# Kernel optimization log

Measured on AMD Instinct MI355X. Metric: run time of the kernel, lower is better.

The kernel has to match this reference:

```python
import jax, jax.numpy as jnp
import numpy as np

B, T, X, H, Z = 64, 2048, 128, 256, 64


def setup_inputs() -> dict:
    key = jax.random.key(0)
    ks = jax.random.split(key, 6)
    s = lambda n: 1.0 / np.sqrt(n).astype(np.float32)
    return {
        "x_seq": jax.random.normal(ks[0], (B, T, X), jnp.float32),
        # LSTMCell params packed as [i|f|g|o] gates. Flax: input dense has no bias,
        # hidden dense has bias.
        "Wi": jax.random.normal(ks[1], (X, 4 * H), jnp.float32) * s(X),
        "Wh": jax.random.normal(ks[2], (H, 4 * H), jnp.float32) * s(H),
        "bh": jnp.zeros((4 * H,), jnp.float32),
        # head: Dense(H) -> relu -> Dense(2Z)
        "W1": jax.random.normal(ks[3], (H, H), jnp.float32) * s(H),
        "b1": jnp.zeros((H,), jnp.float32),
        "W2": jax.random.normal(ks[4], (H, 2 * Z), jnp.float32) * s(H),
        "b2": jnp.zeros((2 * Z,), jnp.float32),
    }


def _forward(x_seq, Wi, Wh, bh, W1, b1, W2, b2):
    Bsz = x_seq.shape[0]
    Hd = Wh.shape[0]
    # Precompute input projection for all timesteps (one big GEMM).
    x_proj = jnp.einsum('btx,xg->btg', x_seq, Wi)  # (B, T, 4H)
    xp = jnp.swapaxes(x_proj, 0, 1)  # (T, B, 4H) for scan

    def step(carry, xp_t):
        c, h = carry
        gates = xp_t + h @ Wh + bh  # (B, 4H)
        i, f, g, o = jnp.split(gates, 4, axis=-1)
        i = jax.nn.sigmoid(i)
        f = jax.nn.sigmoid(f)
        g = jnp.tanh(g)
        o = jax.nn.sigmoid(o)
        c = f * c + i * g
        h = o * jnp.tanh(c)
        hid = jax.nn.relu(h @ W1 + b1)
        out = hid @ W2 + b2  # (B, 2Z)
        return (c, h), out

    c0 = jnp.zeros((Bsz, Hd), x_seq.dtype)
    h0 = jnp.zeros((Bsz, Hd), x_seq.dtype)
    _, outs = jax.lax.scan(step, (c0, h0), xp)  # outs: (T, B, 2Z)
    outs = jnp.swapaxes(outs, 0, 1)  # (B, T, 2Z)
    mu_seq, log_sigma_seq = jnp.split(outs, 2, axis=-1)
    return mu_seq, log_sigma_seq


def reference(x_seq, Wi, Wh, bh, W1, b1, W2, b2):
    return _forward(x_seq, Wi, Wh, bh, W1, b1, W2, b2)
```

## Files before the change

### kernel.cpp

```cpp
#include <hip/hip_runtime.h>

typedef _Float16 f16;
typedef _Float16 h2 __attribute__((ext_vector_type(2)));
typedef _Float16 h8 __attribute__((ext_vector_type(8)));
typedef float f4 __attribute__((ext_vector_type(4)));

constexpr int Bb = 64, Tt = 2048, Xx = 128, Hh = 256, G4 = 1024, Z2 = 128;

__device__ __forceinline__ float fdot2f(h2 a, h2 b, float c) {
#if __has_builtin(__builtin_amdgcn_fdot2)
  return __builtin_amdgcn_fdot2(a, b, c, false);
#else
  return c + (float)a[0] * (float)b[0] + (float)a[1] * (float)b[1];
#endif
}
__device__ __forceinline__ float tanhf_(float x) {
  float e = __expf(2.0f * x);
  return 1.0f - 2.0f * __builtin_amdgcn_rcpf(e + 1.0f);
}
__device__ __forceinline__ h2 bch2(unsigned int u) { return __builtin_bit_cast(h2, u); }

template <int CTRL>
__device__ __forceinline__ float qb(float v) {
  return __builtin_bit_cast(float,
      __builtin_amdgcn_mov_dpp(__builtin_bit_cast(int, v), CTRL, 0xf, 0xf, true));
}
__device__ __forceinline__ float qsum(float v) {
  v += qb<0xB1>(v);
  v += qb<0x4E>(v);
  return v;
}

__global__ void cast_f16_k(const float* __restrict__ in, f16* __restrict__ out, int n) {
  int i = (blockIdx.x * 256 + threadIdx.x) * 4;
  if (i >= n) return;
  float4 v = *(const float4*)(in + i);
  h2 a = {(f16)v.x, (f16)v.y};
  h2 b = {(f16)v.z, (f16)v.w};
  uint2 o = {__builtin_bit_cast(unsigned int, a), __builtin_bit_cast(unsigned int, b)};
  *(uint2*)(out + i) = o;
}

__global__ void cast_whT_k(const float* __restrict__ Wh, f16* __restrict__ WhT) {
  int idx = blockIdx.x * 256 + threadIdx.x;
  int tid = idx >> 8, r = idx & 255;
  int s = r >> 1, e = r & 1;
  int half = s >> 6, gate = (s >> 4) & 3, kk = s & 15;
  int j = tid >> 2, q = tid & 3;
  int k = q * 64 + half * 32 + kk * 2 + e;
  WhT[idx] = (f16)Wh[(long)k * G4 + gate * 256 + j];
}

__global__ void cast_whT2_k(const float* __restrict__ Wh, f16* __restrict__ WhT2) {
  int idx = blockIdx.x * 256 + threadIdx.x;
  int tid = idx >> 9, f = idx & 511;
  int s = f >> 1, e = f & 1;
  int c_off, k;
  if (s < 96)      { c_off = 0; k = 2 * s + e; }
  else if (s < 192){ c_off = 1; k = 2 * (s - 96) + e; }
  else if (s < 224){ c_off = 0; k = 192 + 2 * (s - 192) + e; }
  else             { c_off = 1; k = 192 + 2 * (s - 224) + e; }
  int cc = 2 * tid + c_off;
  int j = cc >> 2, g = cc & 3;
  WhT2[(long)tid * 512 + f] = (f16)Wh[(long)k * G4 + g * 256 + j];
}

__global__ __launch_bounds__(256, 4) void gemm_f16_k(
    const f16* __restrict__ A, const f16* __restrict__ Bm, const float* __restrict__ bias,
    f16* __restrict__ C16, float* __restrict__ Cmu, float* __restrict__ Cls,
    int N, int K, int a_shift, int a_ostride, int a_t0,
    int mode, int o_t0, int tcshift)
{
  __shared__ __align__(16) f16 At[64][48];
  __shared__ __align__(16) f16 Bt[64][48];
  const int tid = threadIdx.x;
  const int mblk = blockIdx.x, nblk = blockIdx.y;
  const int w = tid >> 6, lane = tid & 63;

  const int sa_row = tid >> 2, sa_k = (tid & 3) * 8;
  const int m_g = mblk * 64 + sa_row;
  const long arow = (long)(m_g >> a_shift) * a_ostride + a_t0 + (m_g & ((1 << a_shift) - 1));
  const f16* aptr = A + arow * K + sa_k;
  const int sb_k = tid >> 3, sb_n = (tid & 7) * 8;
  const f16* bptr = Bm + (long)sb_k * N + nblk * 64 + sb_n;

  f4 acc[4];
#pragma unroll
  for (int i = 0; i < 4; ++i) acc[i] = (f4){0.f, 0.f, 0.f, 0.f};

  const int arow_l = w * 16 + (lane & 15);
  const int k0 = (lane >> 4) * 8;

  for (int kk = 0; kk < K; kk += 32) {
    uint4 av = *(const uint4*)(aptr + kk);
    uint4 bv = *(const uint4*)(bptr + (long)kk * N);
    __syncthreads();
    *(uint4*)&At[sa_row][sa_k] = av;
    h8 bx = __builtin_bit_cast(h8, bv);
#pragma unroll
    for (int j = 0; j < 8; ++j) Bt[sb_n + j][sb_k] = bx[j];
    __syncthreads();
    h8 af = *(const h8*)&At[arow_l][k0];
#pragma unroll
    for (int nt = 0; nt < 4; ++nt) {
      h8 bf = *(const h8*)&Bt[nt * 16 + (lane & 15)][k0];
      acc[nt] = __builtin_amdgcn_mfma_f32_16x16x32_f16(af, bf, acc[nt], 0, 0, 0);
    }
  }

  const int row_l = w * 16 + ((lane >> 4) << 2);
  const int col_l = lane & 15;
#pragma unroll
  for (int nt = 0; nt < 4; ++nt) {
    int gcol = nblk * 64 + nt * 16 + col_l;
    float bv = bias[gcol];
#pragma unroll
    for (int r = 0; r < 4; ++r) {
      int gm = mblk * 64 + row_l + r;
      float val = acc[nt][r] + bv;
      if (mode == 1) val = fmaxf(val, 0.f);
      if (mode <= 1) {
        C16[(long)gm * N + gcol] = (f16)val;
      } else {
        int bb = gm >> tcshift, tl = gm & ((1 << tcshift) - 1);
        long orow = (long)bb * Tt + o_t0 + tl;
        if (gcol < 64) Cmu[orow * 64 + gcol] = val;
        else Cls[orow * 64 + (gcol - 64)] = val;
      }
    }
  }
}

__global__ void __launch_bounds__(512, 2) lstm512_k(
    const f16* __restrict__ WhT2, const f16* __restrict__ xp,
    f16* __restrict__ hout, float* __restrict__ c_state, f16* __restrict__ h_state,
    int TC, int first)
{
  const int b = blockIdx.x, tid = threadIdx.x;
  const int j = tid >> 1, odd = tid & 1;
  __shared__ __align__(16) h2 hbuf[2][128];
  __shared__ uint4 wt[16][512];

  h2 w[192];
  {
    const uint4* p4 = (const uint4*)(WhT2 + (long)tid * 512);
#pragma unroll
    for (int u = 0; u < 48; ++u) {
      uint4 v = p4[u];
      w[4 * u + 0] = bch2(v.x); w[4 * u + 1] = bch2(v.y);
      w[4 * u + 2] = bch2(v.z); w[4 * u + 3] = bch2(v.w);
    }
#pragma unroll
    for (int gg = 0; gg < 16; ++gg) wt[gg][tid] = p4[48 + gg];
  }

  float c = first ? 0.f : c_state[b * Hh + j];
  if (tid < 128) {
    h2 hz = {(f16)0.f, (f16)0.f};
    hbuf[0][tid] = first ? hz : ((const h2*)h_state)[b * 128 + tid];
  }
  __syncthreads();

  const float sgn0 = odd ? 2.0f : -1.0f;
  const int xcol0 = (odd * 2) * 256 + j;
  const int xcol1 = xcol0 + 256;
  const f16* xbase = xp + (long)b * TC * G4;
  const f16* xptr0 = xbase + xcol0;
  const f16* xptr1 = xbase + xcol1;
  const f16* xend0 = xptr0 + (long)(TC - 1) * G4;
  f16 xc0 = *xptr0, xc1 = *xptr1;
  int p = 0;
  for (int t = 0; t < TC; ++t) {
    bool last = (xptr0 == xend0);
    const f16* xn0p = last ? xptr0 : xptr0 + G4;
    const f16* xn1p = last ? xptr1 : xptr1 + G4;
    f16 xn0 = *xn0p, xn1 = *xn1p;

    float a0 = (float)xc0, b0 = 0.f, a1 = (float)xc1, b1 = 0.f;
    const uint4* hb4 = (const uint4*)&hbuf[p][0];
#pragma unroll
    for (int i = 0; i < 24; ++i) {
      uint4 hv = hb4[i];
      a0 = fdot2f(w[4 * i + 0], bch2(hv.x), a0);
      b0 = fdot2f(w[4 * i + 1], bch2(hv.y), b0);
      a0 = fdot2f(w[4 * i + 2], bch2(hv.z), a0);
      b0 = fdot2f(w[4 * i + 3], bch2(hv.w), b0);
      a1 = fdot2f(w[96 + 4 * i + 0], bch2(hv.x), a1);
      b1 = fdot2f(w[96 + 4 * i + 1], bch2(hv.y), b1);
      a1 = fdot2f(w[96 + 4 * i + 2], bch2(hv.z), a1);
      b1 = fdot2f(w[96 + 4 * i + 3], bch2(hv.w), b1);
    }
#pragma unroll
    for (int gg = 0; gg < 8; ++gg) {
      uint4 hv = hb4[24 + gg];
      uint4 wa = wt[gg][tid];
      uint4 wb = wt[8 + gg][tid];
      a0 = fdot2f(bch2(wa.x), bch2(hv.x), a0);
      b0 = fdot2f(bch2(wa.y), bch2(hv.y), b0);
      a0 = fdot2f(bch2(wa.z), bch2(hv.z), a0);
      b0 = fdot2f(bch2(wa.w), bch2(hv.w), b0);
      a1 = fdot2f(bch2(wb.x), bch2(hv.x), a1);
      b1 = fdot2f(bch2(wb.y), bch2(hv.y), b1);
      a1 = fdot2f(bch2(wb.z), bch2(hv.z), a1);
      b1 = fdot2f(bch2(wb.w), bch2(hv.w), b1);
    }
    float A0 = a0 + b0, A1 = a1 + b1;

    float e0 = __expf(sgn0 * A0);
    float r0 = __builtin_amdgcn_rcpf(1.0f + e0);
    float act0 = odd ? 1.0f - 2.0f * r0 : r0;
    float e1 = __expf(-A1);
    float act1 = __builtin_amdgcn_rcpf(1.0f + e1);

    float px0 = qb<0xB1>(act0), px1 = qb<0xB1>(act1);
    float ai = odd ? px0 : act0;
    float af = odd ? px1 : act1;
    float ag = odd ? act0 : px0;
    float ao = odd ? act1 : px1;
    c = af * c + ai * ag;
    float hval = ao * tanhf_(c);
    if (!odd) {
      f16 hh = (f16)hval;
      ((f16*)&hbuf[p ^ 1][0])[j] = hh;
      hout[((long)b * TC + t) * Hh + j] = hh;
    }
    __syncthreads();
    p ^= 1;
    xc0 = xn0; xc1 = xn1;
    xptr0 = xn0p; xptr1 = xn1p;
  }
  if (!odd) c_state[b * Hh + j] = c;
  if (tid < 128) ((h2*)h_state)[b * 128 + tid] = hbuf[p][tid];
}

__global__ void __launch_bounds__(1024, 4) lstm_rec_k(
    const f16* __restrict__ WhT, const f16* __restrict__ xp,
    f16* __restrict__ hout, float* __restrict__ c_state, f16* __restrict__ h_state,
    int TC, int first)
{
  const int b = blockIdx.x, tid = threadIdx.x;
  const int j = tid >> 2, q = tid & 3;
  __shared__ __align__(16) h2 hbuf[2][4][36];
  __shared__ __align__(16) h2 wlds[9][1024][4];

  h2 w[92];
  {
    const uint4* p4 = (const uint4*)(WhT + (long)tid * 256);
#pragma unroll
    for (int i = 0; i < 23; ++i) {
      uint4 v = p4[i];
      w[4 * i + 0] = bch2(v.x); w[4 * i + 1] = bch2(v.y);
      w[4 * i + 2] = bch2(v.z); w[4 * i + 3] = bch2(v.w);
    }
#pragma unroll
    for (int gg = 0; gg < 9; ++gg) *(uint4*)&wlds[gg][tid][0] = p4[23 + gg];
  }

  float c = first ? 0.f : c_state[b * Hh + j];
  if (tid < 128) {
    h2 hz = {(f16)0.f, (f16)0.f};
    hbuf[0][tid >> 5][tid & 31] = first ? hz : ((const h2*)h_state)[b * 128 + tid];
  }
  __syncthreads();

  const float sgn = (q == 2) ? 2.0f : -1.0f;
  const int xcol = (q << 8) | j;
  const f16* xptr = xp + (long)b * TC * G4 + xcol;
  const f16* xend = xptr + (long)(TC - 1) * G4;
  f16 xc = *xptr;
  int p = 0;
  for (int t = 0; t < TC; ++t) {
    const f16* xnp = (xptr == xend) ? xptr : xptr + G4;
    f16 xn = *xnp;

    const uint4* hq = (const uint4*)&hbuf[p][q][0];
    float d0 = 0.f, d1 = 0.f, d2 = 0.f, d3 = 0.f;
    {
      uint4 ha = hq[0], hb_ = hq[1], hc = hq[2], hd = hq[3];
      h2 hh0[16] = {bch2(ha.x),  bch2(ha.y),  bch2(ha.z),  bch2(ha.w),
                    bch2(hb_.x), bch2(hb_.y), bch2(hb_.z), bch2(hb_.w),
                    bch2(hc.x),  bch2(hc.y),  bch2(hc.z),  bch2(hc.w),
                    bch2(hd.x),  bch2(hd.y),  bch2(hd.z),  bch2(hd.w)};
#pragma unroll
      for (int m = 0; m < 16; ++m) {
        d0 = fdot2f(w[m], hh0[m], d0);
        d1 = fdot2f(w[16 + m], hh0[m], d1);
        d2 = fdot2f(w[32 + m], hh0[m], d2);
        d3 = fdot2f(w[48 + m], hh0[m], d3);
      }
    }
    {
      uint4 ha = hq[4], hb_ = hq[5], hc = hq[6], hd = hq[7];
      h2 hh1[16] = {bch2(ha.x),  bch2(ha.y),  bch2(ha.z),  bch2(ha.w),
                    bch2(hb_.x), bch2(hb_.y), bch2(hb_.z), bch2(hb_.w),
                    bch2(hc.x),  bch2(hc.y),  bch2(hc.z),  bch2(hc.w),
                    bch2(hd.x),  bch2(hd.y),  bch2(hd.z),  bch2(hd.w)};
#pragma unroll
      for (int m = 0; m < 16; ++m) d0 = fdot2f(w[64 + m], hh1[m], d0);
#pragma unroll
      for (int m = 0; m < 12; ++m) d1 = fdot2f(w[80 + m], hh1[m], d1);
      {
        uint4 wv = *(const uint4*)&wlds[0][tid][0];
        d1 = fdot2f(bch2(wv.x), hh1[12], d1);
        d1 = fdot2f(bch2(wv.y), hh1[13], d1);
        d1 = fdot2f(bch2(wv.z), hh1[14], d1);
        d1 = fdot2f(bch2(wv.w), hh1[15], d1);
      }
#pragma unroll
      for (int gg = 1; gg <= 4; ++gg) {
        uint4 wv = *(const uint4*)&wlds[gg][tid][0];
        int m0 = 4 * (gg - 1);
        d2 = fdot2f(bch2(wv.x), hh1[m0 + 0], d2);
        d2 = fdot2f(bch2(wv.y), hh1[m0 + 1], d2);
        d2 = fdot2f(bch2(wv.z), hh1[m0 + 2], d2);
        d2 = fdot2f(bch2(wv.w), hh1[m0 + 3], d2);
      }
#pragma unroll
      for (int gg = 5; gg <= 8; ++gg) {
        uint4 wv = *(const uint4*)&wlds[gg][tid][0];
        int m0 = 4 * (gg - 5);
        d3 = fdot2f(bch2(wv.x), hh1[m0 + 0], d3);
        d3 = fdot2f(bch2(wv.y), hh1[m0 + 1], d3);
        d3 = fdot2f(bch2(wv.z), hh1[m0 + 2], d3);
        d3 = fdot2f(bch2(wv.w), hh1[m0 + 3], d3);
      }
    }

    d0 = qsum(d0); d1 = qsum(d1); d2 = qsum(d2); d3 = qsum(d3);
    float a = (q & 1) ? d1 : d0;
    float b2_ = (q & 1) ? d3 : d2;
    a = (q & 2) ? b2_ : a;
    a += (float)xc;

    float e = __expf(sgn * a);
    float r = __builtin_amdgcn_rcpf(1.0f + e);
    float act = (q == 2) ? 1.0f - 2.0f * r : r;

    float ai = qb<0x00>(act), af = qb<0x55>(act);
    float ag = qb<0xAA>(act), ao = qb<0xFF>(act);
    c = af * c + ai * ag;
    float hval = ao * tanhf_(c);
    if (q == 3) {
      f16 hh = (f16)hval;
      ((f16*)&hbuf[p ^ 1][0][0])[(j >> 6) * 72 + (j & 63)] = hh;
      hout[((long)b * TC + t) * Hh + j] = hh;
    }
    __syncthreads();
    p ^= 1;
    xc = xn;
    xptr = xnp;
  }
  if (q == 0) c_state[b * Hh + j] = c;
  if (tid < 128) ((h2*)h_state)[b * 128 + tid] = hbuf[p][tid >> 5][tid & 31];
}

extern "C" void kernel_launch(void* const* d_in, const int* in_sizes, int n_in,
                              void* d_out, int out_size, void* d_ws, size_t ws_size,
                              hipStream_t stream)
{
  const float* x  = (const float*)d_in[0];
  const float* Wi = (const float*)d_in[1];
  const float* Wh = (const float*)d_in[2];
  const float* bh = (const float*)d_in[3];
  const float* W1 = (const float*)d_in[4];
  const float* b1 = (const float*)d_in[5];
  const float* W2 = (const float*)d_in[6];
  const float* b2 = (const float*)d_in[7];
  float* out = (float*)d_out;

  char* ws = (char*)d_ws;
  size_t off = 0;
  auto alloc = [&](size_t bytes) -> char* {
    char* p = ws + off;
    off = (off + bytes + 255) & ~(size_t)255;
    return p;
  };
  f16* x16   = (f16*)alloc((size_t)Bb * Tt * Xx * 2);
  f16* wi16  = (f16*)alloc((size_t)Xx * G4 * 2);
  f16* whT16 = (f16*)alloc((size_t)G4 * Hh * 2);
  f16* whT2  = (f16*)alloc((size_t)G4 * Hh * 2);
  f16* w116  = (f16*)alloc((size_t)Hh * Hh * 2);
  f16* w216  = (f16*)alloc((size_t)Hh * Z2 * 2);
  float* cst = (float*)alloc((size_t)Bb * Hh * 4);
  f16* hst   = (f16*)alloc((size_t)Bb * Hh * 2);

  int tc = 1024;
  while (tc > 32) {
    size_t need = (size_t)Bb * tc * G4 * 2 + (size_t)Bb * tc * Hh * 2;
    if (off + need <= ws_size) break;
    tc >>= 1;
  }
  int tcsh = __builtin_ctz((unsigned)tc);
  f16* xp16 = (f16*)alloc((size_t)Bb * tc * G4 * 2);
  f16* h16  = (f16*)alloc((size_t)Bb * tc * Hh * 2);
  f16* hid16 = xp16;

  cast_f16_k<<<(Bb * Tt * Xx) / 1024, 256, 0, stream>>>(x, x16, Bb * Tt * Xx);
  cast_f16_k<<<(Xx * G4) / 1024, 256, 0, stream>>>(Wi, wi16, Xx * G4);
  cast_f16_k<<<(Hh * Hh) / 1024, 256, 0, stream>>>(W1, w116, Hh * Hh);
  cast_f16_k<<<(Hh * Z2) / 1024, 256, 0, stream>>>(W2, w216, Hh * Z2);
  cast_whT_k<<<(Hh * G4) / 256, 256, 0, stream>>>(Wh, whT16);
  cast_whT2_k<<<(Hh * G4) / 256, 256, 0, stream>>>(Wh, whT2);

  float* mu = out;
  float* ls = out + (size_t)Bb * Tt * 64;

  int ci = 0;
  for (int t0 = 0; t0 < Tt; t0 += tc, ++ci) {
    dim3 gx(Bb * tc / 64, G4 / 64);
    gemm_f16_k<<<gx, 256, 0, stream>>>(x16, wi16, bh, xp16, nullptr, nullptr,
                                       G4, Xx, tcsh, Tt, t0, 0, 0, 0);
    if (ci == 0)
      lstm512_k<<<Bb, 512, 0, stream>>>(whT2, xp16, h16, cst, hst, tc, (t0 == 0) ? 1 : 0);
    else
      lstm_rec_k<<<Bb, 1024, 0, stream>>>(whT16, xp16, h16, cst, hst, tc, (t0 == 0) ? 1 : 0);
    dim3 g1g(Bb * tc / 64, Hh / 64);
    gemm_f16_k<<<g1g, 256, 0, stream>>>(h16, w116, b1, hid16, nullptr, nullptr,
                                        Hh, Hh, 30, 0, 0, 1, 0, 0);
    dim3 g2g(Bb * tc / 64, Z2 / 64);
    gemm_f16_k<<<g2g, 256, 0, stream>>>(hid16, w216, b2, nullptr, mu, ls,
                                        Z2, Hh, 30, 0, 0, 2, t0, tcsh);
  }
}
```

Baseline: 3.354 ms.

## Add K-split LSTM recurrence kernel with two threads per hidden unit

Adds a new recurrent kernel in which each hidden unit is handled by two threads, each owning half of the K dimension for all four gates. Each thread computes its four gate activations directly, so only one cross-lane add is needed instead of a quad reduction plus activation broadcast. The first chunk uses the new kernel, later chunks fall back to the older 512-thread kernel, and the 1024-thread variant is removed. Each thread now evaluates all four gate nonlinearities redundantly, and weights still spill partly into LDS.

```diff
diff --git a/kernel.cpp b/kernel.cpp
--- a/kernel.cpp
+++ b/kernel.cpp
@@ -24,11 +24,6 @@
 __device__ __forceinline__ float qb(float v) {
   return __builtin_bit_cast(float,
       __builtin_amdgcn_mov_dpp(__builtin_bit_cast(int, v), CTRL, 0xf, 0xf, true));
-}
-__device__ __forceinline__ float qsum(float v) {
-  v += qb<0xB1>(v);
-  v += qb<0x4E>(v);
-  return v;
 }
 
 __global__ void cast_f16_k(const float* __restrict__ in, f16* __restrict__ out, int n) {
@@ -39,16 +34,6 @@
   h2 b = {(f16)v.z, (f16)v.w};
   uint2 o = {__builtin_bit_cast(unsigned int, a), __builtin_bit_cast(unsigned int, b)};
   *(uint2*)(out + i) = o;
-}
-
-__global__ void cast_whT_k(const float* __restrict__ Wh, f16* __restrict__ WhT) {
-  int idx = blockIdx.x * 256 + threadIdx.x;
-  int tid = idx >> 8, r = idx & 255;
-  int s = r >> 1, e = r & 1;
-  int half = s >> 6, gate = (s >> 4) & 3, kk = s & 15;
-  int j = tid >> 2, q = tid & 3;
-  int k = q * 64 + half * 32 + kk * 2 + e;
-  WhT[idx] = (f16)Wh[(long)k * G4 + gate * 256 + j];
 }
 
 __global__ void cast_whT2_k(const float* __restrict__ Wh, f16* __restrict__ WhT2) {
@@ -65,6 +50,16 @@
   WhT2[(long)tid * 512 + f] = (f16)Wh[(long)k * G4 + g * 256 + j];
 }
 
+__global__ void cast_whT4_k(const float* __restrict__ Wh, f16* __restrict__ WhT4) {
+  int idx = blockIdx.x * 256 + threadIdx.x;
+  int tid = idx >> 9, f = idx & 511;
+  int s = f >> 1, e = f & 1;
+  int i = s >> 4, g = (s >> 2) & 3, m = s & 3;
+  int j = tid >> 1, hf = tid & 1;
+  int k = 128 * hf + 8 * i + 2 * m + e;
+  WhT4[(long)tid * 512 + f] = (f16)Wh[(long)k * G4 + g * 256 + j];
+}
+
 __global__ __launch_bounds__(256, 4) void gemm_f16_k(
     const f16* __restrict__ A, const f16* __restrict__ Bm, const float* __restrict__ bias,
     f16* __restrict__ C16, float* __restrict__ Cmu, float* __restrict__ Cls,
@@ -129,6 +124,102 @@
       }
     }
   }
+}
+
+__global__ void __launch_bounds__(512, 2) lstm512h_k(
+    const f16* __restrict__ WhT4, const f16* __restrict__ xp,
+    f16* __restrict__ hout, float* __restrict__ c_state, f16* __restrict__ h_state,
+    int TC, int first)
+{
+  const int b = blockIdx.x, tid = threadIdx.x;
+  const int j = tid >> 1, hf = tid & 1;
+  __shared__ __align__(16) h2 hbuf[2][128];
+  __shared__ uint4 wt[16][512];
+
+  h2 w[192];
+  {
+    const uint4* p4 = (const uint4*)(WhT4 + (long)tid * 512);
+#pragma unroll
+    for (int u = 0; u < 48; ++u) {
+      uint4 v = p4[u];
+      w[4 * u + 0] = bch2(v.x); w[4 * u + 1] = bch2(v.y);
+      w[4 * u + 2] = bch2(v.z); w[4 * u + 3] = bch2(v.w);
+    }
+#pragma unroll
+    for (int gg = 0; gg < 16; ++gg) wt[gg][tid] = p4[48 + gg];
+  }
+
+  float c = first ? 0.f : c_state[b * Hh + j];
+  if (tid < 128) {
+    h2 hz = {(f16)0.f, (f16)0.f};
+    hbuf[0][tid] = first ? hz : ((const h2*)h_state)[b * 128 + tid];
+  }
+  __syncthreads();
+
+  const f16* xptr = xp + (long)b * TC * G4 + j;
+  const f16* xend = xptr + (long)(TC - 1) * G4;
+  f16 xc0 = xptr[0], xc1 = xptr[256], xc2 = xptr[512], xc3 = xptr[768];
+  int p = 0;
+  for (int t = 0; t < TC; ++t) {
+    const f16* xnp = (xptr == xend) ? xptr : xptr + G4;
+    f16 xn0 = xnp[0], xn1 = xnp[256], xn2 = xnp[512], xn3 = xnp[768];
+
+    float d0 = 0.f, d1 = 0.f, d2 = 0.f, d3 = 0.f;
+    const uint4* hq = (const uint4*)&hbuf[p][0] + hf * 16;
+#pragma unroll
+    for (int i = 0; i < 12; ++i) {
+      uint4 hv = hq[i];
+      h2 h0 = bch2(hv.x), h1 = bch2(hv.y), h2_ = bch2(hv.z), h3 = bch2(hv.w);
+      d0 = fdot2f(w[16 * i + 0], h0, d0);  d0 = fdot2f(w[16 * i + 1], h1, d0);
+      d0 = fdot2f(w[16 * i + 2], h2_, d0); d0 = fdot2f(w[16 * i + 3], h3, d0);
+      d1 = fdot2f(w[16 * i + 4], h0, d1);  d1 = fdot2f(w[16 * i + 5], h1, d1);
+      d1 = fdot2f(w[16 * i + 6], h2_, d1); d1 = fdot2f(w[16 * i + 7], h3, d1);
+      d2 = fdot2f(w[16 * i + 8], h0, d2);  d2 = fdot2f(w[16 * i + 9], h1, d2);
+      d2 = fdot2f(w[16 * i + 10], h2_, d2); d2 = fdot2f(w[16 * i + 11], h3, d2);
+      d3 = fdot2f(w[16 * i + 12], h0, d3);  d3 = fdot2f(w[16 * i + 13], h1, d3);
+      d3 = fdot2f(w[16 * i + 14], h2_, d3); d3 = fdot2f(w[16 * i + 15], h3, d3);
+    }
+#pragma unroll
+    for (int i = 12; i < 16; ++i) {
+      uint4 hv = hq[i];
+      h2 h0 = bch2(hv.x), h1 = bch2(hv.y), h2_ = bch2(hv.z), h3 = bch2(hv.w);
+      uint4 w0 = wt[(i - 12) * 4 + 0][tid];
+      uint4 w1 = wt[(i - 12) * 4 + 1][tid];
+      uint4 w2 = wt[(i - 12) * 4 + 2][tid];
+      uint4 w3 = wt[(i - 12) * 4 + 3][tid];
+      d0 = fdot2f(bch2(w0.x), h0, d0); d0 = fdot2f(bch2(w0.y), h1, d0);
+      d0 = fdot2f(bch2(w0.z), h2_, d0); d0 = fdot2f(bch2(w0.w), h3, d0);
+      d1 = fdot2f(bch2(w1.x), h0, d1); d1 = fdot2f(bch2(w1.y), h1, d1);
+      d1 = fdot2f(bch2(w1.z), h2_, d1); d1 = fdot2f(bch2(w1.w), h3, d1);
+      d2 = fdot2f(bch2(w2.x), h0, d2); d2 = fdot2f(bch2(w2.y), h1, d2);
+      d2 = fdot2f(bch2(w2.z), h2_, d2); d2 = fdot2f(bch2(w2.w), h3, d2);
+      d3 = fdot2f(bch2(w3.x), h0, d3); d3 = fdot2f(bch2(w3.y), h1, d3);
+      d3 = fdot2f(bch2(w3.z), h2_, d3); d3 = fdot2f(bch2(w3.w), h3, d3);
+    }
+
+    d0 += qb<0xB1>(d0); d1 += qb<0xB1>(d1);
+    d2 += qb<0xB1>(d2); d3 += qb<0xB1>(d3);
+
+    float ti = d0 + (float)xc0, tf = d1 + (float)xc1;
+    float tg = d2 + (float)xc2, to = d3 + (float)xc3;
+    float ai = __builtin_amdgcn_rcpf(1.0f + __expf(-ti));
+    float af = __builtin_amdgcn_rcpf(1.0f + __expf(-tf));
+    float ag = 1.0f - 2.0f * __builtin_amdgcn_rcpf(1.0f + __expf(2.0f * tg));
+    float ao = __builtin_amdgcn_rcpf(1.0f + __expf(-to));
+    c = af * c + ai * ag;
+    float hval = ao * tanhf_(c);
+    if (!hf) {
+      f16 hh = (f16)hval;
+      ((f16*)&hbuf[p ^ 1][0])[j] = hh;
+      hout[((long)b * TC + t) * Hh + j] = hh;
+    }
+    __syncthreads();
+    p ^= 1;
+    xc0 = xn0; xc1 = xn1; xc2 = xn2; xc3 = xn3;
+    xptr = xnp;
+  }
+  if (!hf) c_state[b * Hh + j] = c;
+  if (tid < 128) ((h2*)h_state)[b * 128 + tid] = hbuf[p][tid];
 }
 
 __global__ void __launch_bounds__(512, 2) lstm512_k(
@@ -233,127 +324,6 @@
   if (tid < 128) ((h2*)h_state)[b * 128 + tid] = hbuf[p][tid];
 }
 
-__global__ void __launch_bounds__(1024, 4) lstm_rec_k(
-    const f16* __restrict__ WhT, const f16* __restrict__ xp,
-    f16* __restrict__ hout, float* __restrict__ c_state, f16* __restrict__ h_state,
-    int TC, int first)
-{
-  const int b = blockIdx.x, tid = threadIdx.x;
-  const int j = tid >> 2, q = tid & 3;
-  __shared__ __align__(16) h2 hbuf[2][4][36];
-  __shared__ __align__(16) h2 wlds[9][1024][4];
-
-  h2 w[92];
-  {
-    const uint4* p4 = (const uint4*)(WhT + (long)tid * 256);
-#pragma unroll
-    for (int i = 0; i < 23; ++i) {
-      uint4 v = p4[i];
-      w[4 * i + 0] = bch2(v.x); w[4 * i + 1] = bch2(v.y);
-      w[4 * i + 2] = bch2(v.z); w[4 * i + 3] = bch2(v.w);
-    }
-#pragma unroll
-    for (int gg = 0; gg < 9; ++gg) *(uint4*)&wlds[gg][tid][0] = p4[23 + gg];
-  }
-
-  float c = first ? 0.f : c_state[b * Hh + j];
-  if (tid < 128) {
-    h2 hz = {(f16)0.f, (f16)0.f};
-    hbuf[0][tid >> 5][tid & 31] = first ? hz : ((const h2*)h_state)[b * 128 + tid];
-  }
-  __syncthreads();
-
-  const float sgn = (q == 2) ? 2.0f : -1.0f;
-  const int xcol = (q << 8) | j;
-  const f16* xptr = xp + (long)b * TC * G4 + xcol;
-  const f16* xend = xptr + (long)(TC - 1) * G4;
-  f16 xc = *xptr;
-  int p = 0;
-  for (int t = 0; t < TC; ++t) {
-    const f16* xnp = (xptr == xend) ? xptr : xptr + G4;
-    f16 xn = *xnp;
-
-    const uint4* hq = (const uint4*)&hbuf[p][q][0];
-    float d0 = 0.f, d1 = 0.f, d2 = 0.f, d3 = 0.f;
-    {
-      uint4 ha = hq[0], hb_ = hq[1], hc = hq[2], hd = hq[3];
-      h2 hh0[16] = {bch2(ha.x),  bch2(ha.y),  bch2(ha.z),  bch2(ha.w),
-                    bch2(hb_.x), bch2(hb_.y), bch2(hb_.z), bch2(hb_.w),
-                    bch2(hc.x),  bch2(hc.y),  bch2(hc.z),  bch2(hc.w),
-                    bch2(hd.x),  bch2(hd.y),  bch2(hd.z),  bch2(hd.w)};
-#pragma unroll
-      for (int m = 0; m < 16; ++m) {
-        d0 = fdot2f(w[m], hh0[m], d0);
-        d1 = fdot2f(w[16 + m], hh0[m], d1);
-        d2 = fdot2f(w[32 + m], hh0[m], d2);
-        d3 = fdot2f(w[48 + m], hh0[m], d3);
-      }
-    }
-    {
-      uint4 ha = hq[4], hb_ = hq[5], hc = hq[6], hd = hq[7];
-      h2 hh1[16] = {bch2(ha.x),  bch2(ha.y),  bch2(ha.z),  bch2(ha.w),
-                    bch2(hb_.x), bch2(hb_.y), bch2(hb_.z), bch2(hb_.w),
-                    bch2(hc.x),  bch2(hc.y),  bch2(hc.z),  bch2(hc.w),
-                    bch2(hd.x),  bch2(hd.y),  bch2(hd.z),  bch2(hd.w)};
-#pragma unroll
-      for (int m = 0; m < 16; ++m) d0 = fdot2f(w[64 + m], hh1[m], d0);
-#pragma unroll
-      for (int m = 0; m < 12; ++m) d1 = fdot2f(w[80 + m], hh1[m], d1);
-      {
-        uint4 wv = *(const uint4*)&wlds[0][tid][0];
-        d1 = fdot2f(bch2(wv.x), hh1[12], d1);
-        d1 = fdot2f(bch2(wv.y), hh1[13], d1);
-        d1 = fdot2f(bch2(wv.z), hh1[14], d1);
-        d1 = fdot2f(bch2(wv.w), hh1[15], d1);
-      }
-#pragma unroll
-      for (int gg = 1; gg <= 4; ++gg) {
-        uint4 wv = *(const uint4*)&wlds[gg][tid][0];
-        int m0 = 4 * (gg - 1);
-        d2 = fdot2f(bch2(wv.x), hh1[m0 + 0], d2);
-        d2 = fdot2f(bch2(wv.y), hh1[m0 + 1], d2);
-        d2 = fdot2f(bch2(wv.z), hh1[m0 + 2], d2);
-        d2 = fdot2f(bch2(wv.w), hh1[m0 + 3], d2);
-      }
-#pragma unroll
-      for (int gg = 5; gg <= 8; ++gg) {
-        uint4 wv = *(const uint4*)&wlds[gg][tid][0];
-        int m0 = 4 * (gg - 5);
-        d3 = fdot2f(bch2(wv.x), hh1[m0 + 0], d3);
-        d3 = fdot2f(bch2(wv.y), hh1[m0 + 1], d3);
-        d3 = fdot2f(bch2(wv.z), hh1[m0 + 2], d3);
-        d3 = fdot2f(bch2(wv.w), hh1[m0 + 3], d3);
-      }
-    }
-
-    d0 = qsum(d0); d1 = qsum(d1); d2 = qsum(d2); d3 = qsum(d3);
-    float a = (q & 1) ? d1 : d0;
-    float b2_ = (q & 1) ? d3 : d2;
-    a = (q & 2) ? b2_ : a;
-    a += (float)xc;
-
-    float e = __expf(sgn * a);
-    float r = __builtin_amdgcn_rcpf(1.0f + e);
-    float act = (q == 2) ? 1.0f - 2.0f * r : r;
-
-    float ai = qb<0x00>(act), af = qb<0x55>(act);
-    float ag = qb<0xAA>(act), ao = qb<0xFF>(act);
-    c = af * c + ai * ag;
-    float hval = ao * tanhf_(c);
-    if (q == 3) {
-      f16 hh = (f16)hval;
-      ((f16*)&hbuf[p ^ 1][0][0])[(j >> 6) * 72 + (j & 63)] = hh;
-      hout[((long)b * TC + t) * Hh + j] = hh;
-    }
-    __syncthreads();
-    p ^= 1;
-    xc = xn;
-    xptr = xnp;
-  }
-  if (q == 0) c_state[b * Hh + j] = c;
-  if (tid < 128) ((h2*)h_state)[b * 128 + tid] = hbuf[p][tid >> 5][tid & 31];
-}
-
 extern "C" void kernel_launch(void* const* d_in, const int* in_sizes, int n_in,
                               void* d_out, int out_size, void* d_ws, size_t ws_size,
                               hipStream_t stream)
@@ -377,8 +347,8 @@
   };
   f16* x16   = (f16*)alloc((size_t)Bb * Tt * Xx * 2);
   f16* wi16  = (f16*)alloc((size_t)Xx * G4 * 2);
-  f16* whT16 = (f16*)alloc((size_t)G4 * Hh * 2);
   f16* whT2  = (f16*)alloc((size_t)G4 * Hh * 2);
+  f16* whT4  = (f16*)alloc((size_t)G4 * Hh * 2);
   f16* w116  = (f16*)alloc((size_t)Hh * Hh * 2);
   f16* w216  = (f16*)alloc((size_t)Hh * Z2 * 2);
   float* cst = (float*)alloc((size_t)Bb * Hh * 4);
@@ -399,8 +369,8 @@
   cast_f16_k<<<(Xx * G4) / 1024, 256, 0, stream>>>(Wi, wi16, Xx * G4);
   cast_f16_k<<<(Hh * Hh) / 1024, 256, 0, stream>>>(W1, w116, Hh * Hh);
   cast_f16_k<<<(Hh * Z2) / 1024, 256, 0, stream>>>(W2, w216, Hh * Z2);
-  cast_whT_k<<<(Hh * G4) / 256, 256, 0, stream>>>(Wh, whT16);
   cast_whT2_k<<<(Hh * G4) / 256, 256, 0, stream>>>(Wh, whT2);
+  cast_whT4_k<<<(Hh * G4) / 256, 256, 0, stream>>>(Wh, whT4);
 
   float* mu = out;
   float* ls = out + (size_t)Bb * Tt * 64;
@@ -411,9 +381,9 @@
     gemm_f16_k<<<gx, 256, 0, stream>>>(x16, wi16, bh, xp16, nullptr, nullptr,
                                        G4, Xx, tcsh, Tt, t0, 0, 0, 0);
     if (ci == 0)
+      lstm512h_k<<<Bb, 512, 0, stream>>>(whT4, xp16, h16, cst, hst, tc, (t0 == 0) ? 1 : 0);
+    else
       lstm512_k<<<Bb, 512, 0, stream>>>(whT2, xp16, h16, cst, hst, tc, (t0 == 0) ? 1 : 0);
-    else
-      lstm_rec_k<<<Bb, 1024, 0, stream>>>(whT16, xp16, h16, cst, hst, tc, (t0 == 0) ? 1 : 0);
     dim3 g1g(Bb * tc / 64, Hh / 64);
     gemm_f16_k<<<g1g, 256, 0, stream>>>(h16, w116, b1, hid16, nullptr, nullptr,
                                         Hh, Hh, 30, 0, 0, 1, 0, 0);
```

Measured after the change: 3.224 ms. -3.9%, faster.
